# Kernel optimization log

Measured on AMD Instinct MI355X. Metric: run time of the kernel, lower is better.

## Reference

```python
import jax, jax.numpy as jnp
import numpy as np

N_NODES = 100000
N_EDGES = 1600000
N_GRAPHS = 64
IN_DIM = 128
HID = 64
N_CLASSES = 10


def setup_inputs() -> dict:
    key = jax.random.key(0)
    ks = jax.random.split(key, 8)
    x = jax.random.normal(ks[0], (N_NODES, IN_DIM), jnp.float32)
    edge_index = jax.random.randint(ks[1], (2, N_EDGES), 0, N_NODES, jnp.int32)
    graph_id = jnp.sort(jax.random.randint(ks[2], (N_NODES,), 0, N_GRAPHS, jnp.int32))
    W1 = jax.random.normal(ks[3], (IN_DIM, HID), jnp.float32) / np.sqrt(IN_DIM)
    b1 = jnp.zeros((HID,), jnp.float32)
    W2 = jax.random.normal(ks[4], (HID, HID), jnp.float32) / np.sqrt(HID)
    b2 = jnp.zeros((HID,), jnp.float32)
    attn_W = jax.random.normal(ks[5], (HID, 1), jnp.float32) / np.sqrt(HID)
    attn_b = jnp.zeros((1,), jnp.float32)
    cls_W = jax.random.normal(ks[6], (HID, N_CLASSES), jnp.float32) / np.sqrt(HID)
    cls_b = jnp.zeros((N_CLASSES,), jnp.float32)
    return {"x": x, "edge_index": edge_index, "graph_id": graph_id,
            "W1": W1, "b1": b1, "W2": W2, "b2": b2,
            "attn_W": attn_W, "attn_b": attn_b, "cls_W": cls_W, "cls_b": cls_b}


def _graph_conv(h, W, b, src, dst, norm_out, norm_in):
    # DGL GraphConv, norm='both': D_in^{-1/2} A D_out^{-1/2} (h W) + b
    h = h @ W                                  # [N, out]
    h = h * norm_out[:, None]                  # scale by src out-degree^{-1/2}
    m = jax.ops.segment_sum(h[src], dst, num_segments=N_NODES)  # SpMM aggregation
    return m * norm_in[:, None] + b


def reference(x, edge_index, graph_id, W1, b1, W2, b2, attn_W, attn_b, cls_W, cls_b):
    src, dst = edge_index[0], edge_index[1]
    ones_e = jnp.ones((src.shape[0],), jnp.float32)
    deg_out = jnp.clip(jax.ops.segment_sum(ones_e, src, num_segments=N_NODES), 1.0)
    deg_in = jnp.clip(jax.ops.segment_sum(ones_e, dst, num_segments=N_NODES), 1.0)
    norm_out = jax.lax.rsqrt(deg_out)
    norm_in = jax.lax.rsqrt(deg_in)

    h = jax.nn.relu(_graph_conv(x, W1, b1, src, dst, norm_out, norm_in))
    h = jax.nn.relu(_graph_conv(h, W2, b2, src, dst, norm_out, norm_in))

    hw = jax.nn.sigmoid(h @ attn_W + attn_b)   # [N, 1] attention gate
    h = h * hw

    # mean_nodes: per-graph mean pooling
    sums = jax.ops.segment_sum(h, graph_id, num_segments=N_GRAPHS)        # [G, HID]
    cnts = jnp.clip(jax.ops.segment_sum(jnp.ones((N_NODES,), jnp.float32), graph_id,
                                        num_segments=N_GRAPHS), 1.0)
    hg = sums / cnts[:, None]
    out = hg @ cls_W + cls_b                   # [G, n_classes]
    return out, hw
```

## Files before the change

### kernel.cpp

```cpp
#include <hip/hip_runtime.h>
#include <stdint.h>


#define N_NODES   100000
#define N_EDGES   1600000
#define N_GRAPHS  64
#define IN_DIM    128
#define HID       64
#define N_CLASSES 10

#define NBUCK     391
#define P1B       196
#define EPB       8192
#define GB_BLOCKS 391
#define GEMM_BLOCKS 782
#define SPMM_BLOCKS 3125
#define POOL_SLICES 32
#define WS_NEED   33885952u

__device__ __forceinline__ float bf2f(unsigned short u) {
  unsigned int v = ((unsigned int)u) << 16;
  float f;
  __builtin_memcpy(&f, &v, 4);
  return f;
}

__device__ __forceinline__ unsigned short f2bf(float f) {
  unsigned int x;
  __builtin_memcpy(&x, &f, 4);
  unsigned int lsb = (x >> 16) & 1u;
  x += 0x7fffu + lsb;
  return (unsigned short)(x >> 16);
}

__device__ __forceinline__ void unpack_bf2(unsigned int u, float& lo, float& hi) {
  unsigned int a = u << 16;
  unsigned int b = u & 0xffff0000u;
  __builtin_memcpy(&lo, &a, 4);
  __builtin_memcpy(&hi, &b, 4);
}

__device__ __forceinline__ float ldf(const void* p, int i, int mode) {
  return mode ? bf2f(((const unsigned short*)p)[i]) : ((const float*)p)[i];
}

__global__ __launch_bounds__(256) void probe_kernel(const unsigned short* __restrict__ xu,
                                                    int* __restrict__ flag) {
  int tid = (int)threadIdx.x;
  unsigned u = xu[2 * tid];
  int e = (int)((u >> 7) & 0xFF);
  int ok = (e >= 110 && e <= 132) ? 1 : 0;
  unsigned long long m = __ballot(ok);
  __shared__ int cnt[4];
  if ((tid & 63) == 0) cnt[tid >> 6] = __popcll(m);
  __syncthreads();
  if (tid == 0) {
    flag[0] = (cnt[0] + cnt[1] + cnt[2] + cnt[3] > 128) ? 1 : 0;
    flag[1] = 1;
  }
}

__global__ __launch_bounds__(256) void fallback_kernel(unsigned short* __restrict__ out,
                                                       int n) {
  int i = blockIdx.x * 256 + threadIdx.x;
  if (i < n) out[i] = 0;
}

__global__ __launch_bounds__(256) void wcvt_kernel(
    const void* __restrict__ W1, const void* __restrict__ W2,
    const void* __restrict__ b1, const void* __restrict__ b2,
    const void* __restrict__ attnW, const void* __restrict__ attnb,
    const void* __restrict__ clsW, const void* __restrict__ clsb,
    float* __restrict__ Wf1, float* __restrict__ Wf2,
    float* __restrict__ b1f, float* __restrict__ b2f,
    float* __restrict__ attnWf, float* __restrict__ attnbf,
    float* __restrict__ clsWf, float* __restrict__ clsbf,
    const int* __restrict__ flag) {
  int mode = flag[0];
  int i = blockIdx.x * 256 + threadIdx.x;
  if (i < IN_DIM * HID) Wf1[i] = ldf(W1, i, mode);
  if (i < HID * HID)    Wf2[i] = ldf(W2, i, mode);
  if (i < HID) {
    b1f[i] = ldf(b1, i, mode);
    b2f[i] = ldf(b2, i, mode);
    attnWf[i] = ldf(attnW, i, mode);
  }
  if (i == 0) attnbf[0] = ldf(attnb, 0, mode);
  if (i < HID * N_CLASSES) clsWf[i] = ldf(clsW, i, mode);
  if (i < N_CLASSES) clsbf[i] = ldf(clsb, i, mode);
}

__global__ __launch_bounds__(256) void part_count_kernel(
    const int* __restrict__ ei, int* __restrict__ blkhistD,
    int* __restrict__ blkhistS,
    const int* __restrict__ gid, int* __restrict__ gstart) {
  int b = (int)blockIdx.x;
  int t = (int)threadIdx.x;
  if (b < P1B) {
    __shared__ int hD[NBUCK];
    __shared__ int hS[NBUCK];
    for (int i = t; i < NBUCK; i += 256) { hD[i] = 0; hS[i] = 0; }
    __syncthreads();
    int base_e = b * EPB;
    for (int s = 0; s < EPB / 1024; ++s) {
      int e4 = base_e + s * 1024 + t * 4;
      if (e4 < N_EDGES) {
        int4 s4 = *(const int4*)(ei + e4);
        int4 d4 = *(const int4*)(ei + N_EDGES + e4);
        int ss[4] = {s4.x, s4.y, s4.z, s4.w};
        int dd[4] = {d4.x, d4.y, d4.z, d4.w};
#pragma unroll
        for (int j = 0; j < 4; ++j) {
          if ((unsigned)ss[j] < N_NODES) atomicAdd(&hS[ss[j] >> 8], 1);
          if ((unsigned)dd[j] < N_NODES) atomicAdd(&hD[dd[j] >> 8], 1);
        }
      }
    }
    __syncthreads();
    for (int i = t; i < NBUCK; i += 256) {
      blkhistD[b * NBUCK + i] = hD[i];
      blkhistS[b * NBUCK + i] = hS[i];
    }
  } else {
    int bb = b - P1B;
    int n = bb * 256 + t;
    if (n >= N_NODES) return;
    int gc = gid[n] & (N_GRAPHS - 1);
    if (n == 0) {
      for (int g = 0; g <= gc; ++g) gstart[g] = 0;
    } else {
      int gp = gid[n - 1] & (N_GRAPHS - 1);
      for (int g = gp + 1; g <= gc; ++g) gstart[g] = n;
    }
    if (n == N_NODES - 1) {
      for (int g = gc + 1; g <= N_GRAPHS; ++g) gstart[g] = N_NODES;
    }
  }
}

__global__ __launch_bounds__(512) void bucket_scan_kernel(
    int* __restrict__ blkhistD, int* __restrict__ blkhistS,
    int* __restrict__ bstart_d, int* __restrict__ bstart_s) {
  int* hist = (blockIdx.x == 0) ? blkhistD : blkhistS;
  int* bst  = (blockIdx.x == 0) ? bstart_d : bstart_s;
  int u = (int)threadIdx.x;
  int tot = 0;
  if (u < NBUCK) {
    for (int blk = 0; blk < P1B; ++blk) tot += hist[blk * NBUCK + u];
  }
  __shared__ int smA[512];
  __shared__ int smB[512];
  smA[u] = tot;
  __syncthreads();
  int* a = smA;
  int* bq = smB;
  for (int off = 1; off < 512; off <<= 1) {
    int v = a[u];
    if (u >= off) v += a[u - off];
    bq[u] = v;
    __syncthreads();
    int* tmp = a; a = bq; bq = tmp;
  }
  int excl = a[u] - tot;
  if (u <= NBUCK) bst[u] = excl;
  if (u < NBUCK) {
    int off2 = excl;
    for (int blk = 0; blk < P1B; ++blk) {
      int h = hist[blk * NBUCK + u];
      hist[blk * NBUCK + u] = off2;
      off2 += h;
    }
  }
}

__global__ __launch_bounds__(256) void part_scatter_kernel(
    const int* __restrict__ ei, const int* __restrict__ blkbaseD,
    const int* __restrict__ blkbaseS,
    int2* __restrict__ edst, int* __restrict__ esrc) {
  __shared__ int cD[NBUCK];
  __shared__ int cS[NBUCK];
  int b = (int)blockIdx.x;
  int t = (int)threadIdx.x;
  for (int i = t; i < NBUCK; i += 256) {
    cD[i] = blkbaseD[b * NBUCK + i];
    cS[i] = blkbaseS[b * NBUCK + i];
  }
  __syncthreads();
  int base_e = b * EPB;
  for (int s = 0; s < EPB / 1024; ++s) {
    int e4 = base_e + s * 1024 + t * 4;
    if (e4 < N_EDGES) {
      int4 s4 = *(const int4*)(ei + e4);
      int4 d4 = *(const int4*)(ei + N_EDGES + e4);
      int ss[4] = {s4.x, s4.y, s4.z, s4.w};
      int dd[4] = {d4.x, d4.y, d4.z, d4.w};
#pragma unroll
      for (int j = 0; j < 4; ++j) {
        if ((unsigned)ss[j] < N_NODES) {
          int slot = atomicAdd(&cS[ss[j] >> 8], 1);
          esrc[slot] = ss[j];
        }
        if ((unsigned)dd[j] < N_NODES) {
          int slot = atomicAdd(&cD[dd[j] >> 8], 1);
          edst[slot] = make_int2(ss[j], dd[j]);
        }
      }
    }
  }
}

__global__ __launch_bounds__(256) void csr_kernel(
    const int2* __restrict__ edst, const int* __restrict__ esrc,
    const int* __restrict__ bstart_d, const int* __restrict__ bstart_s,
    int* __restrict__ rowptr, int* __restrict__ colx,
    float* __restrict__ norm_in, float* __restrict__ norm_out) {
  __shared__ int lc[256];
  __shared__ int smA[256];
  __shared__ int smB[256];
  int b = (int)blockIdx.x;
  int t = (int)threadIdx.x;
  if (b < NBUCK) {
    int node0 = b << 8;
    int base = bstart_d[b];
    int end  = bstart_d[b + 1];
    lc[t] = 0;
    __syncthreads();
    for (int i = base + t; i < end; i += 256) {
      int2 p = edst[i];
      atomicAdd(&lc[p.y - node0], 1);
    }
    __syncthreads();
    int my = lc[t];
    smA[t] = my;
    __syncthreads();
    int* a = smA;
    int* bq = smB;
    for (int off = 1; off < 256; off <<= 1) {
      int v = a[t];
      if (t >= off) v += a[t - off];
      bq[t] = v;
      __syncthreads();
      int* tmp = a; a = bq; bq = tmp;
    }
    int excl = a[t] - my;
    int n = node0 + t;
    if (n <= N_NODES) rowptr[n] = base + excl;
    if (n < N_NODES) {
      int c = my < 1 ? 1 : my;
      norm_in[n] = rsqrtf((float)c);
    }
    __syncthreads();
    lc[t] = base + excl;
    __syncthreads();
    for (int i = base + t; i < end; i += 256) {
      int2 p = edst[i];
      int slot = atomicAdd(&lc[p.y - node0], 1);
      colx[slot] = p.x;
    }
  } else {
    int bb = b - NBUCK;
    int node0 = bb << 8;
    int base = bstart_s[bb];
    int end  = bstart_s[bb + 1];
    lc[t] = 0;
    __syncthreads();
    for (int i = base + t; i < end; i += 256) {
      atomicAdd(&lc[esrc[i] - node0], 1);
    }
    __syncthreads();
    int n = node0 + t;
    if (n < N_NODES) {
      int c = lc[t] < 1 ? 1 : lc[t];
      norm_out[n] = rsqrtf((float)c);
    }
  }
}

template <int K>
__global__ __launch_bounds__(256) void gemm_kernel(const void* __restrict__ A,
                                                   const float* __restrict__ Wf,
                                                   const float* __restrict__ norm_out,
                                                   unsigned short* __restrict__ out,
                                                   const int* __restrict__ flag) {
  int mode = flag[0];
  int n = blockIdx.x * 128 + ((int)threadIdx.x & 127);
  int d0 = __builtin_amdgcn_readfirstlane((int)((threadIdx.x >> 7) << 5));
  if (n >= N_NODES) return;
  float acc[32];
#pragma unroll
  for (int i = 0; i < 32; ++i) acc[i] = 0.f;
  if (mode) {
    const unsigned short* xr = (const unsigned short*)A + (size_t)n * K;
    for (int k0 = 0; k0 < K; k0 += 8) {
      uint4 xv = *(const uint4*)(xr + k0);
      float xf[8];
      unpack_bf2(xv.x, xf[0], xf[1]);
      unpack_bf2(xv.y, xf[2], xf[3]);
      unpack_bf2(xv.z, xf[4], xf[5]);
      unpack_bf2(xv.w, xf[6], xf[7]);
#pragma unroll
      for (int j = 0; j < 8; ++j) {
        const float* wrow = Wf + (k0 + j) * HID + d0;
#pragma unroll
        for (int d = 0; d < 32; ++d) acc[d] += xf[j] * wrow[d];
      }
    }
  } else {
    const float* xr = (const float*)A + (size_t)n * K;
    for (int k0 = 0; k0 < K; k0 += 8) {
      float4 a0 = *(const float4*)(xr + k0);
      float4 a1 = *(const float4*)(xr + k0 + 4);
      float xf[8] = {a0.x, a0.y, a0.z, a0.w, a1.x, a1.y, a1.z, a1.w};
#pragma unroll
      for (int j = 0; j < 8; ++j) {
        const float* wrow = Wf + (k0 + j) * HID + d0;
#pragma unroll
        for (int d = 0; d < 32; ++d) acc[d] += xf[j] * wrow[d];
      }
    }
  }
  float s = norm_out[n];
  unsigned short* orow = out + (size_t)n * HID + d0;
#pragma unroll
  for (int d = 0; d < 32; ++d) orow[d] = f2bf(acc[d] * s);
}

__device__ __forceinline__ void accum8(uint4 v, float acc[8]) {
  float lo, hi;
  unpack_bf2(v.x, lo, hi); acc[0] += lo; acc[1] += hi;
  unpack_bf2(v.y, lo, hi); acc[2] += lo; acc[3] += hi;
  unpack_bf2(v.z, lo, hi); acc[4] += lo; acc[5] += hi;
  unpack_bf2(v.w, lo, hi); acc[6] += lo; acc[7] += hi;
}

__device__ __forceinline__ void spmm_gather8(const unsigned short* __restrict__ hs,
                                             const int* __restrict__ col,
                                             int e0, int e1, int dim0,
                                             float acc[8]) {
  int e = e0;
  for (; e + 4 <= e1; e += 4) {
    unsigned c0 = (unsigned)col[e];
    unsigned c1 = (unsigned)col[e + 1];
    unsigned c2 = (unsigned)col[e + 2];
    unsigned c3 = (unsigned)col[e + 3];
    uint4 v0 = make_uint4(0u, 0u, 0u, 0u);
    uint4 v1 = v0, v2 = v0, v3 = v0;
    if (c0 < N_NODES) v0 = *(const uint4*)(hs + ((size_t)c0 << 6) + dim0);
    if (c1 < N_NODES) v1 = *(const uint4*)(hs + ((size_t)c1 << 6) + dim0);
    if (c2 < N_NODES) v2 = *(const uint4*)(hs + ((size_t)c2 << 6) + dim0);
    if (c3 < N_NODES) v3 = *(const uint4*)(hs + ((size_t)c3 << 6) + dim0);
    accum8(v0, acc);
    accum8(v1, acc);
    accum8(v2, acc);
    accum8(v3, acc);
  }
  for (; e < e1; ++e) {
    unsigned c = (unsigned)col[e];
    uint4 v = make_uint4(0u, 0u, 0u, 0u);
    if (c < N_NODES) v = *(const uint4*)(hs + ((size_t)c << 6) + dim0);
    accum8(v, acc);
  }
}

__global__ __launch_bounds__(256) void spmm_kernel(const unsigned short* __restrict__ hs,
                                                   const int* __restrict__ rowptr,
                                                   const int* __restrict__ col,
                                                   const float* __restrict__ norm_in,
                                                   const float* __restrict__ b1f,
                                                   unsigned short* __restrict__ out) {
  int n = (int)(blockIdx.x * 32 + (threadIdx.x >> 3));
  int dim0 = ((int)threadIdx.x & 7) << 3;
  if (n >= N_NODES) return;
  int e0 = rowptr[n], e1 = rowptr[n + 1];
  if (e0 < 0) e0 = 0;
  if (e1 > N_EDGES) e1 = N_EDGES;
  float acc[8];
#pragma unroll
  for (int i = 0; i < 8; ++i) acc[i] = 0.f;
  spmm_gather8(hs, col, e0, e1, dim0, acc);
  float nin = norm_in[n];
  unsigned int pk[4];
#pragma unroll
  for (int i = 0; i < 4; ++i) {
    float vlo = fmaxf(acc[2 * i] * nin + b1f[dim0 + 2 * i], 0.f);
    float vhi = fmaxf(acc[2 * i + 1] * nin + b1f[dim0 + 2 * i + 1], 0.f);
    pk[i] = (unsigned int)f2bf(vlo) | ((unsigned int)f2bf(vhi) << 16);
  }
  *(uint4*)(out + ((size_t)n << 6) + dim0) = make_uint4(pk[0], pk[1], pk[2], pk[3]);
}

__global__ __launch_bounds__(256) void spmm_attn_kernel(
    const unsigned short* __restrict__ hs,
    const int* __restrict__ rowptr, const int* __restrict__ col,
    const float* __restrict__ norm_in, const float* __restrict__ b2f,
    const float* __restrict__ attnWf, const float* __restrict__ attnbf,
    void* __restrict__ out_base, unsigned short* __restrict__ gated,
    const int* __restrict__ flag) {
  int mode = flag[0];
  int n = (int)(blockIdx.x * 32 + (threadIdx.x >> 3));
  int dim0 = ((int)threadIdx.x & 7) << 3;
  if (n >= N_NODES) return;
  int e0 = rowptr[n], e1 = rowptr[n + 1];
  if (e0 < 0) e0 = 0;
  if (e1 > N_EDGES) e1 = N_EDGES;
  float acc[8];
#pragma unroll
  for (int i = 0; i < 8; ++i) acc[i] = 0.f;
  spmm_gather8(hs, col, e0, e1, dim0, acc);
  float nin = norm_in[n];
  float vv[8];
  float p = 0.f;
#pragma unroll
  for (int i = 0; i < 8; ++i) {
    vv[i] = fmaxf(acc[i] * nin + b2f[dim0 + i], 0.f);
    p += vv[i] * attnWf[dim0 + i];
  }
#pragma unroll
  for (int m = 1; m <= 4; m <<= 1) p += __shfl_xor(p, m, 64);
  float logit = p + attnbf[0];
  float hwv = 1.f / (1.f + __expf(-logit));
  if ((threadIdx.x & 7) == 0) {
    if (mode) ((unsigned short*)out_base)[N_GRAPHS * N_CLASSES + n] = f2bf(hwv);
    else      ((float*)out_base)[N_GRAPHS * N_CLASSES + n] = hwv;
  }
  unsigned int pk[4];
#pragma unroll
  for (int i = 0; i < 4; ++i) {
    pk[i] = (unsigned int)f2bf(vv[2 * i] * hwv) |
            ((unsigned int)f2bf(vv[2 * i + 1] * hwv) << 16);
  }
  *(uint4*)(gated + ((size_t)n << 6) + dim0) = make_uint4(pk[0], pk[1], pk[2], pk[3]);
}

__global__ __launch_bounds__(256) void pool_kernel(const unsigned short* __restrict__ gated,
                                                   const int* __restrict__ gstart,
                                                   float* __restrict__ gpart) {
  int g = (int)blockIdx.x >> 5;
  int s = (int)blockIdx.x & 31;
  int dim = (int)threadIdx.x & 63;
  int rsel = (int)threadIdx.x >> 6;
  int r0 = gstart[g], r1 = gstart[g + 1];
  if (r0 < 0) r0 = 0;
  if (r1 > N_NODES) r1 = N_NODES;
  int len = r1 - r0;
  if (len < 0) len = 0;
  int a = r0 + (int)(((long long)len * s) >> 5);
  int bnd = r0 + (int)(((long long)len * (s + 1)) >> 5);
  float acc = 0.f;
  for (int r = a + rsel; r < bnd; r += 4)
    acc += bf2f(gated[((size_t)r << 6) + dim]);
  __shared__ float sm[256];
  sm[threadIdx.x] = acc;
  __syncthreads();
  if (threadIdx.x < 64)
    gpart[((size_t)blockIdx.x << 6) + dim] =
        sm[dim] + sm[64 + dim] + sm[128 + dim] + sm[192 + dim];
}

__global__ __launch_bounds__(64) void pool_reduce_kernel(const float* __restrict__ gpart,
                                                         float* __restrict__ gsum) {
  int g = (int)blockIdx.x;
  int dim = (int)threadIdx.x;
  float acc = 0.f;
#pragma unroll
  for (int s = 0; s < POOL_SLICES; ++s)
    acc += gpart[(((size_t)g << 5) + s << 6) + dim];
  gsum[((size_t)g << 6) + dim] = acc;
}

__global__ __launch_bounds__(640) void final_kernel(const float* __restrict__ gsum,
                                                    const int* __restrict__ gstart,
                                                    const float* __restrict__ clsWf,
                                                    const float* __restrict__ clsbf,
                                                    void* __restrict__ out_base,
                                                    const int* __restrict__ flag) {
  int mode = flag[0];
  int t = (int)threadIdx.x;
  if (t >= N_GRAPHS * N_CLASSES) return;
  int g = t / N_CLASSES, c = t - g * N_CLASSES;
  int cg = gstart[g + 1] - gstart[g];
  if (cg < 1) cg = 1;
  float inv = 1.f / (float)cg;
  float acc = 0.f;
#pragma unroll
  for (int d = 0; d < HID; ++d) acc += gsum[(g << 6) + d] * clsWf[d * N_CLASSES + c];
  float r = acc * inv + clsbf[c];
  if (mode) ((unsigned short*)out_base)[t] = f2bf(r);
  else      ((float*)out_base)[t] = r;
}

extern "C" void kernel_launch(void* const* d_in, const int* in_sizes, int n_in,
                              void* d_out, int out_size, void* d_ws, size_t ws_size,
                              hipStream_t stream) {
  const void* x     = d_in[0];
  const int*  ei    = (const int*)d_in[1];
  const int*  gid   = (const int*)d_in[2];
  const void* W1    = d_in[3];
  const void* b1    = d_in[4];
  const void* W2    = d_in[5];
  const void* b2    = d_in[6];
  const void* attnW = d_in[7];
  const void* attnb = d_in[8];
  const void* clsW  = d_in[9];
  const void* clsb  = d_in[10];

  if (ws_size < (size_t)WS_NEED) {
    fallback_kernel<<<(out_size + 255) / 256, 256, 0, stream>>>(
        (unsigned short*)d_out, out_size);
    return;
  }

  char* w = (char*)d_ws;
  int*   flag     = (int*)(w + 0);
  int*   gstart   = (int*)(w + 64);
  float* gsum     = (float*)(w + 576);
  int*   bstart_d = (int*)(w + 16960);
  int*   bstart_s = (int*)(w + 18560);
  int*   blkhD    = (int*)(w + 20160);
  int*   blkhS    = (int*)(w + 326720);
  int*   rowptr   = (int*)(w + 633280);
  float* norm_out = (float*)(w + 1033344);
  float* norm_in  = (float*)(w + 1433344);
  float* Wf1      = (float*)(w + 1833344);
  float* Wf2      = (float*)(w + 1866112);
  float* b1f      = (float*)(w + 1882496);
  float* b2f      = (float*)(w + 1882752);
  float* attnWf   = (float*)(w + 1883008);
  float* attnbf   = (float*)(w + 1883264);
  float* clsWf    = (float*)(w + 1883328);
  float* clsbf    = (float*)(w + 1885888);
  int*   colx     = (int*)(w + 1885952);
  int2*  edst     = (int2*)(w + 8285952);
  int*   esrc     = (int*)(w + 21085952);
  unsigned short* bufA = (unsigned short*)(w + 8285952);
  unsigned short* bufB = (unsigned short*)(w + 21085952);
  float* gpart    = (float*)(w + 20160);

  probe_kernel<<<1, 256, 0, stream>>>((const unsigned short*)x, flag);
  wcvt_kernel<<<32, 256, 0, stream>>>(W1, W2, b1, b2, attnW, attnb, clsW, clsb,
                                      Wf1, Wf2, b1f, b2f, attnWf, attnbf, clsWf,
                                      clsbf, flag);

  part_count_kernel<<<P1B + GB_BLOCKS, 256, 0, stream>>>(ei, blkhD, blkhS, gid, gstart);
  bucket_scan_kernel<<<2, 512, 0, stream>>>(blkhD, blkhS, bstart_d, bstart_s);
  part_scatter_kernel<<<P1B, 256, 0, stream>>>(ei, blkhD, blkhS, edst, esrc);
  csr_kernel<<<2 * NBUCK, 256, 0, stream>>>(edst, esrc, bstart_d, bstart_s,
                                            rowptr, colx, norm_in, norm_out);

  gemm_kernel<IN_DIM><<<GEMM_BLOCKS, 256, 0, stream>>>(x, Wf1, norm_out, bufA, flag);
  spmm_kernel<<<SPMM_BLOCKS, 256, 0, stream>>>(bufA, rowptr, colx, norm_in, b1f, bufB);

  gemm_kernel<HID><<<GEMM_BLOCKS, 256, 0, stream>>>(bufB, Wf2, norm_out, bufA, flag + 1);
  spmm_attn_kernel<<<SPMM_BLOCKS, 256, 0, stream>>>(
      bufA, rowptr, colx, norm_in, b2f, attnWf, attnbf, d_out, bufB, flag);

  pool_kernel<<<N_GRAPHS * POOL_SLICES, 256, 0, stream>>>(bufB, gstart, gpart);
  pool_reduce_kernel<<<N_GRAPHS, 64, 0, stream>>>(gpart, gsum);
  final_kernel<<<1, 640, 0, stream>>>(gsum, gstart, clsWf, clsbf, d_out, flag);
}
```

Before: 297.8 us.

## Replace scalar FMA node GEMMs with bf16 MFMA using hi/lo split precision

The two dense node-feature GEMMs move from per-thread scalar FMA loops to 16x16x32 bf16 MFMA instructions, one wavefront per 16-row tile. To keep near-fp32 accuracy, the weights are split into bf16 high and low parts, pre-swizzled into MFMA fragment layout by the conversion kernel. fp32 activations are split the same way, giving three MFMA passes per k-tile. This targets ALU-bound GEMM time. It costs extra MFMA work and uncoalesced 2-byte output stores, and the split gives slightly different rounding than fp32.

After: 274.7 us. 7.8% less time.

```diff
diff --git a/kernel.cpp b/kernel.cpp
--- a/kernel.cpp
+++ b/kernel.cpp
@@ -13,10 +13,20 @@
 #define P1B       196
 #define EPB       8192
 #define GB_BLOCKS 391
-#define GEMM_BLOCKS 782
+#define MTILES    6250
+#define GEMM_BLOCKS 1563
 #define SPMM_BLOCKS 3125
 #define POOL_SLICES 32
 #define WS_NEED   33885952u
+
+typedef __attribute__((ext_vector_type(8))) short short8v;
+typedef __attribute__((ext_vector_type(4))) float f32x4;
+typedef __bf16 bf16x8 __attribute__((ext_vector_type(8)));
+
+__device__ __forceinline__ f32x4 mfma16(short8v a, short8v b, f32x4 c) {
+  return __builtin_amdgcn_mfma_f32_16x16x32_bf16(
+      __builtin_bit_cast(bf16x8, a), __builtin_bit_cast(bf16x8, b), c, 0, 0, 0);
+}
 
 __device__ __forceinline__ float bf2f(unsigned short u) {
   unsigned int v = ((unsigned int)u) << 16;
@@ -71,15 +81,42 @@
     const void* __restrict__ b1, const void* __restrict__ b2,
     const void* __restrict__ attnW, const void* __restrict__ attnb,
     const void* __restrict__ clsW, const void* __restrict__ clsb,
-    float* __restrict__ Wf1, float* __restrict__ Wf2,
+    unsigned short* __restrict__ W1hf, unsigned short* __restrict__ W1lf,
+    unsigned short* __restrict__ W2hf, unsigned short* __restrict__ W2lf,
     float* __restrict__ b1f, float* __restrict__ b2f,
     float* __restrict__ attnWf, float* __restrict__ attnbf,
     float* __restrict__ clsWf, float* __restrict__ clsbf,
     const int* __restrict__ flag) {
   int mode = flag[0];
   int i = blockIdx.x * 256 + threadIdx.x;
-  if (i < IN_DIM * HID) Wf1[i] = ldf(W1, i, mode);
-  if (i < HID * HID)    Wf2[i] = ldf(W2, i, mode);
+  if (i < 1024) {
+    int tile = i >> 6, lane = i & 63;
+    int kt = tile >> 2, ct = tile & 3;
+#pragma unroll
+    for (int j = 0; j < 8; ++j) {
+      int k = kt * 32 + ((lane >> 4) << 3) + j;
+      int d = (ct << 4) + (lane & 15);
+      float v = ldf(W1, k * HID + d, mode);
+      unsigned short h = f2bf(v);
+      unsigned short l = f2bf(v - bf2f(h));
+      W1hf[i * 8 + j] = h;
+      W1lf[i * 8 + j] = l;
+    }
+  } else if (i < 1536) {
+    int ii = i - 1024;
+    int tile = ii >> 6, lane = ii & 63;
+    int kt = tile >> 2, ct = tile & 3;
+#pragma unroll
+    for (int j = 0; j < 8; ++j) {
+      int k = kt * 32 + ((lane >> 4) << 3) + j;
+      int d = (ct << 4) + (lane & 15);
+      float v = ldf(W2, k * HID + d, mode);
+      unsigned short h = f2bf(v);
+      unsigned short l = f2bf(v - bf2f(h));
+      W2hf[ii * 8 + j] = h;
+      W2lf[ii * 8 + j] = l;
+    }
+  }
   if (i < HID) {
     b1f[i] = ldf(b1, i, mode);
     b2f[i] = ldf(b2, i, mode);
@@ -277,52 +314,82 @@
 }
 
 template <int K>
-__global__ __launch_bounds__(256) void gemm_kernel(const void* __restrict__ A,
-                                                   const float* __restrict__ Wf,
-                                                   const float* __restrict__ norm_out,
-                                                   unsigned short* __restrict__ out,
-                                                   const int* __restrict__ flag) {
+__global__ __launch_bounds__(256) void gemm_mfma_kernel(
+    const void* __restrict__ A, const unsigned short* __restrict__ Whf,
+    const unsigned short* __restrict__ Wlf, const float* __restrict__ norm_out,
+    unsigned short* __restrict__ out, const int* __restrict__ flag) {
   int mode = flag[0];
-  int n = blockIdx.x * 128 + ((int)threadIdx.x & 127);
-  int d0 = __builtin_amdgcn_readfirstlane((int)((threadIdx.x >> 7) << 5));
-  if (n >= N_NODES) return;
-  float acc[32];
-#pragma unroll
-  for (int i = 0; i < 32; ++i) acc[i] = 0.f;
+  int mtile = (int)blockIdx.x * 4 + ((int)threadIdx.x >> 6);
+  if (mtile >= MTILES) return;
+  int n0 = mtile << 4;
+  int lane = (int)threadIdx.x & 63;
+  int row = lane & 15;
+  int kg = lane >> 4;
+  f32x4 acc0 = {0.f, 0.f, 0.f, 0.f};
+  f32x4 acc1 = {0.f, 0.f, 0.f, 0.f};
+  f32x4 acc2 = {0.f, 0.f, 0.f, 0.f};
+  f32x4 acc3 = {0.f, 0.f, 0.f, 0.f};
+  const short8v* whb0 = (const short8v*)Whf + lane;
+  const short8v* wlb0 = (const short8v*)Wlf + lane;
   if (mode) {
-    const unsigned short* xr = (const unsigned short*)A + (size_t)n * K;
-    for (int k0 = 0; k0 < K; k0 += 8) {
-      uint4 xv = *(const uint4*)(xr + k0);
-      float xf[8];
-      unpack_bf2(xv.x, xf[0], xf[1]);
-      unpack_bf2(xv.y, xf[2], xf[3]);
-      unpack_bf2(xv.z, xf[4], xf[5]);
-      unpack_bf2(xv.w, xf[6], xf[7]);
+    const unsigned short* xr = (const unsigned short*)A + (size_t)(n0 + row) * K + (kg << 3);
+#pragma unroll
+    for (int kt = 0; kt < K / 32; ++kt) {
+      uint4 va = *(const uint4*)(xr + kt * 32);
+      short8v xh = __builtin_bit_cast(short8v, va);
+      const short8v* wh = whb0 + (size_t)(kt * 4) * 64;
+      const short8v* wl = wlb0 + (size_t)(kt * 4) * 64;
+      acc0 = mfma16(xh, wh[0], acc0);
+      acc1 = mfma16(xh, wh[64], acc1);
+      acc2 = mfma16(xh, wh[128], acc2);
+      acc3 = mfma16(xh, wh[192], acc3);
+      acc0 = mfma16(xh, wl[0], acc0);
+      acc1 = mfma16(xh, wl[64], acc1);
+      acc2 = mfma16(xh, wl[128], acc2);
+      acc3 = mfma16(xh, wl[192], acc3);
+    }
+  } else {
+    const float* xr = (const float*)A + (size_t)(n0 + row) * K + (kg << 3);
+#pragma unroll
+    for (int kt = 0; kt < K / 32; ++kt) {
+      float4 a0 = *(const float4*)(xr + kt * 32);
+      float4 a1 = *(const float4*)(xr + kt * 32 + 4);
+      float xv[8] = {a0.x, a0.y, a0.z, a0.w, a1.x, a1.y, a1.z, a1.w};
+      short8v xh, xl;
 #pragma unroll
       for (int j = 0; j < 8; ++j) {
-        const float* wrow = Wf + (k0 + j) * HID + d0;
-#pragma unroll
-        for (int d = 0; d < 32; ++d) acc[d] += xf[j] * wrow[d];
+        unsigned short h = f2bf(xv[j]);
+        unsigned short l = f2bf(xv[j] - bf2f(h));
+        xh[j] = (short)h;
+        xl[j] = (short)l;
       }
-    }
-  } else {
-    const float* xr = (const float*)A + (size_t)n * K;
-    for (int k0 = 0; k0 < K; k0 += 8) {
-      float4 a0 = *(const float4*)(xr + k0);
-      float4 a1 = *(const float4*)(xr + k0 + 4);
-      float xf[8] = {a0.x, a0.y, a0.z, a0.w, a1.x, a1.y, a1.z, a1.w};
-#pragma unroll
-      for (int j = 0; j < 8; ++j) {
-        const float* wrow = Wf + (k0 + j) * HID + d0;
-#pragma unroll
-        for (int d = 0; d < 32; ++d) acc[d] += xf[j] * wrow[d];
-      }
-    }
-  }
-  float s = norm_out[n];
-  unsigned short* orow = out + (size_t)n * HID + d0;
-#pragma unroll
-  for (int d = 0; d < 32; ++d) orow[d] = f2bf(acc[d] * s);
+      const short8v* wh = whb0 + (size_t)(kt * 4) * 64;
+      const short8v* wl = wlb0 + (size_t)(kt * 4) * 64;
+      acc0 = mfma16(xh, wh[0], acc0);
+      acc1 = mfma16(xh, wh[64], acc1);
+      acc2 = mfma16(xh, wh[128], acc2);
+      acc3 = mfma16(xh, wh[192], acc3);
+      acc0 = mfma16(xh, wl[0], acc0);
+      acc1 = mfma16(xh, wl[64], acc1);
+      acc2 = mfma16(xh, wl[128], acc2);
+      acc3 = mfma16(xh, wl[192], acc3);
+      acc0 = mfma16(xl, wh[0], acc0);
+      acc1 = mfma16(xl, wh[64], acc1);
+      acc2 = mfma16(xl, wh[128], acc2);
+      acc3 = mfma16(xl, wh[192], acc3);
+    }
+  }
+  int col = lane & 15;
+#pragma unroll
+  for (int i = 0; i < 4; ++i) {
+    int n = n0 + (kg << 2) + i;
+    float s = norm_out[n];
+    size_t rb = (size_t)n << 6;
+    out[rb + col]      = f2bf(acc0[i] * s);
+    out[rb + 16 + col] = f2bf(acc1[i] * s);
+    out[rb + 32 + col] = f2bf(acc2[i] * s);
+    out[rb + 48 + col] = f2bf(acc3[i] * s);
+  }
 }
 
 __device__ __forceinline__ void accum8(uint4 v, float acc[8]) {
@@ -521,8 +588,10 @@
   int*   rowptr   = (int*)(w + 633280);
   float* norm_out = (float*)(w + 1033344);
   float* norm_in  = (float*)(w + 1433344);
-  float* Wf1      = (float*)(w + 1833344);
-  float* Wf2      = (float*)(w + 1866112);
+  unsigned short* W1hf = (unsigned short*)(w + 1833344);
+  unsigned short* W1lf = (unsigned short*)(w + 1849728);
+  unsigned short* W2hf = (unsigned short*)(w + 1866112);
+  unsigned short* W2lf = (unsigned short*)(w + 1874304);
   float* b1f      = (float*)(w + 1882496);
   float* b2f      = (float*)(w + 1882752);
   float* attnWf   = (float*)(w + 1883008);
@@ -538,8 +607,8 @@
 
   probe_kernel<<<1, 256, 0, stream>>>((const unsigned short*)x, flag);
   wcvt_kernel<<<32, 256, 0, stream>>>(W1, W2, b1, b2, attnW, attnb, clsW, clsb,
-                                      Wf1, Wf2, b1f, b2f, attnWf, attnbf, clsWf,
-                                      clsbf, flag);
+                                      W1hf, W1lf, W2hf, W2lf, b1f, b2f, attnWf,
+                                      attnbf, clsWf, clsbf, flag);
 
   part_count_kernel<<<P1B + GB_BLOCKS, 256, 0, stream>>>(ei, blkhD, blkhS, gid, gstart);
   bucket_scan_kernel<<<2, 512, 0, stream>>>(blkhD, blkhS, bstart_d, bstart_s);
@@ -547,10 +616,12 @@
   csr_kernel<<<2 * NBUCK, 256, 0, stream>>>(edst, esrc, bstart_d, bstart_s,
                                             rowptr, colx, norm_in, norm_out);
 
-  gemm_kernel<IN_DIM><<<GEMM_BLOCKS, 256, 0, stream>>>(x, Wf1, norm_out, bufA, flag);
+  gemm_mfma_kernel<IN_DIM><<<GEMM_BLOCKS, 256, 0, stream>>>(
+      x, W1hf, W1lf, norm_out, bufA, flag);
   spmm_kernel<<<SPMM_BLOCKS, 256, 0, stream>>>(bufA, rowptr, colx, norm_in, b1f, bufB);
 
-  gemm_kernel<HID><<<GEMM_BLOCKS, 256, 0, stream>>>(bufB, Wf2, norm_out, bufA, flag + 1);
+  gemm_mfma_kernel<HID><<<GEMM_BLOCKS, 256, 0, stream>>>(
+      bufB, W2hf, W2lf, norm_out, bufA, flag + 1);
   spmm_attn_kernel<<<SPMM_BLOCKS, 256, 0, stream>>>(
       bufA, rowptr, colx, norm_in, b2f, attnWf, attnbf, d_out, bufB, flag);
 
```
